# Performance work log

Measured on AMD Instinct MI355X. Metric: run time of the kernel, lower is better.

Reference implementation:

```python
import jax, jax.numpy as jnp
import numpy as np

N = 50000          # nodes
E = 1000000        # edges
EMB = 64           # emb_dim
L = 3              # num_layer
B = 250            # graphs (200 nodes each)
XF, EF = 7, 5      # node / edge feature dims
BN_EPS = 1e-5


def setup_inputs() -> dict:
    key = jax.random.key(0)
    ks = jax.random.split(key, 16)
    x = jax.random.normal(ks[0], (N, XF), dtype=jnp.float32)
    edge_attr = jax.random.normal(ks[1], (E, EF), dtype=jnp.float32)
    edge_index = jax.random.randint(ks[2], (2, E), 0, N, dtype=jnp.int32)
    # 250 contiguous graphs of 200 nodes: last node index of each graph
    last_idx = jnp.arange(1, B + 1, dtype=jnp.int32) * (N // B) - 1
    s = 0.05
    xW = jax.random.normal(ks[3], (XF, EMB), dtype=jnp.float32) * s
    xb = jnp.zeros((EMB,), dtype=jnp.float32)
    eW = jax.random.normal(ks[4], (L, EF, EMB), dtype=jnp.float32) * s
    eb = jnp.zeros((L, EMB), dtype=jnp.float32)
    W1 = jax.random.normal(ks[5], (L, EMB, 2 * EMB), dtype=jnp.float32) * s
    b1 = jnp.zeros((L, 2 * EMB), dtype=jnp.float32)
    W2 = jax.random.normal(ks[6], (L, 2 * EMB, EMB), dtype=jnp.float32) * s
    b2 = jnp.zeros((L, EMB), dtype=jnp.float32)
    gamma = jnp.ones((L, EMB), dtype=jnp.float32)
    beta = jnp.zeros((L, EMB), dtype=jnp.float32)
    return {"x": x, "edge_attr": edge_attr, "edge_index": edge_index,
            "last_idx": last_idx, "xW": xW, "xb": xb, "eW": eW, "eb": eb,
            "W1": W1, "b1": b1, "W2": W2, "b2": b2,
            "gamma": gamma, "beta": beta}


def _gnn_forward(x, edge_attr, edge_index, last_idx, xW, xb, eW, eb, W1, b1, W2, b2, gamma, beta):
    n = x.shape[0]
    # self-loop edge attrs: first column = 8, rest 0
    self_attr = jnp.zeros((n, EF), dtype=edge_attr.dtype).at[:, 0].set(8.0)
    ea = jnp.concatenate([edge_attr, self_attr], axis=0)          # [E+N, EF]
    loop = jnp.arange(n, dtype=edge_index.dtype)
    src = jnp.concatenate([edge_index[0], loop])                  # x_j indices
    dst = jnp.concatenate([edge_index[1], loop])                  # aggregation targets

    h = x @ xW + xb                                               # [N, EMB]
    for l in range(L):
        e = ea @ eW[l] + eb[l]                                    # [E+N, EMB]
        msg = h[src] + e                                          # gather + combine
        agg = jax.ops.segment_sum(msg, dst, num_segments=n)       # scatter-add
        h2 = jax.nn.relu(agg @ W1[l] + b1[l]) @ W2[l] + b2[l]     # GIN MLP
        mean = jnp.mean(h2, axis=0)
        var = jnp.mean(jnp.square(h2 - mean), axis=0)             # biased, like torch BN
        hn = (h2 - mean) * jax.lax.rsqrt(var + BN_EPS) * gamma[l] + beta[l]
        h = jax.nn.elu(hn) if l < L - 1 else hn                   # drop_ratio = 0
    return h[last_idx]                                            # super-node reps [B, EMB]


def reference(x, edge_attr, edge_index, last_idx, xW, xb, eW, eb, W1, b1, W2, b2, gamma, beta):
    return _gnn_forward(x, edge_attr, edge_index, last_idx, xW, xb, eW, eb, W1, b1, W2, b2, gamma, beta)
```

## Files before the change

### kernel.cpp

```cpp
#include <hip/hip_runtime.h>

#define N_NODES 50000
#define N_EDGES 1000000
#define EMB     64
#define HID     128
#define NLAYER  3
#define NGRAPH  250
#define XFD     7
#define EFD     5
#define BN_EPS  1e-5f

#define BKT_SH 8
#define BKT_SZ 256
#define NBKT   ((N_NODES + BKT_SZ - 1) / BKT_SZ)
#define CHKE   4096
#define NCHK   ((N_EDGES + CHKE - 1) / CHKE)
#define CNTM   (NBKT * NCHK)
#define INPB   ((((N_NODES + 1) * EMB) + 255) / 256)
#define PACKB  ((NLAYER * 2 * EMB * HID + 255) / 256)

typedef short bf8_t __attribute__((ext_vector_type(8)));
typedef float f4_t  __attribute__((ext_vector_type(4)));

union FragU {
    uint4 q;
    bf8_t v;
    unsigned short u[8];
};

__device__ __forceinline__ void atomAddF(float* p, float v) {
    __hip_atomic_fetch_add(p, v, __ATOMIC_RELAXED, __HIP_MEMORY_SCOPE_AGENT);
}

__device__ __forceinline__ unsigned short f2bf(float f) {
    unsigned int u = __float_as_uint(f);
    u += 0x7fffu + ((u >> 16) & 1u);
    return (unsigned short)(u >> 16);
}
__device__ __forceinline__ float bf2f(unsigned short s) {
    return __uint_as_float(((unsigned int)s) << 16);
}
__device__ __forceinline__ float4 bf4(ushort4 u) {
    return make_float4(bf2f(u.x), bf2f(u.y), bf2f(u.z), bf2f(u.w));
}

__global__ void k_prep(const float* __restrict__ x, const float* __restrict__ xW,
                       const float* __restrict__ xb, unsigned short* __restrict__ h,
                       const float* __restrict__ W1, const float* __restrict__ W2,
                       unsigned short* __restrict__ pw1, unsigned short* __restrict__ pw2,
                       float* __restrict__ stats) {
    int bid = blockIdx.x;
    if (bid < INPB) {
        int gid = bid * 256 + threadIdx.x;
        if (gid >= (N_NODES + 1) * EMB) return;
        int n = gid >> 6, f = gid & 63;
        if (n == N_NODES) { h[gid] = 0; return; }
        float acc = xb[f];
#pragma unroll
        for (int k = 0; k < XFD; ++k) acc = fmaf(x[n * XFD + k], xW[k * EMB + f], acc);
        h[gid] = f2bf(acc);
    } else if (bid < INPB + PACKB) {
        int gid = (bid - INPB) * 256 + threadIdx.x;
        int layer = gid >> 14;
        int r = gid & 16383;
        if (layer >= NLAYER) return;
        if (r < 8192) {
            int p = r;
            int j = p & 7, lane = (p >> 3) & 63, ts = p >> 9;
            int t = ts >> 1, s = ts & 1;
            int k = 32 * s + 8 * (lane >> 4) + j;
            int n = 16 * t + (lane & 15);
            pw1[layer * 8192 + p] = f2bf(W1[layer * EMB * HID + k * HID + n]);
        } else {
            int p = r - 8192;
            int j = p & 7, lane = (p >> 3) & 63, ts = p >> 9;
            int t = ts >> 2, s = ts & 3;
            int k = 32 * s + 8 * (lane >> 4) + j;
            int n = 16 * t + (lane & 15);
            pw2[layer * 8192 + p] = f2bf(W2[layer * HID * EMB + k * EMB + n]);
        }
    } else {
        for (int i = threadIdx.x; i < NLAYER * 2 * EMB; i += 256) stats[i] = 0.f;
    }
}

__global__ __launch_bounds__(256) void k_binA(const int* __restrict__ dst,
                                              int* __restrict__ cntmat) {
    __shared__ int hist[NBKT];
    int tid = threadIdx.x, c = blockIdx.x;
    for (int i = tid; i < NBKT; i += 256) hist[i] = 0;
    __syncthreads();
    int e0 = c * CHKE, e1 = min(e0 + CHKE, N_EDGES);
    for (int i = e0 + tid; i < e1; i += 256) atomicAdd(&hist[dst[i] >> BKT_SH], 1);
    __syncthreads();
    for (int b = tid; b < NBKT; b += 256) cntmat[b * NCHK + c] = hist[b];
}

__global__ __launch_bounds__(1024) void k_scan(const int* __restrict__ in,
                                               int* __restrict__ out) {
    __shared__ int wsum[16];
    int tid = threadIdx.x, lane = tid & 63, wid = tid >> 6;
    int carry = 0;
    const int4* in4 = (const int4*)in;
    int4* out4 = (int4*)out;
    const int n4 = CNTM / 4;
    for (int base = 0; base < n4; base += 1024) {
        int i = base + tid;
        int4 v = make_int4(0, 0, 0, 0);
        if (i < n4) v = in4[i];
        int t = v.x + v.y + v.z + v.w;
        int x = t;
#pragma unroll
        for (int off = 1; off < 64; off <<= 1) {
            int y = __shfl_up(x, off);
            if (lane >= off) x += y;
        }
        if (lane == 63) wsum[wid] = x;
        __syncthreads();
        int woff = 0, tot = 0;
#pragma unroll
        for (int w = 0; w < 16; ++w) {
            int s = wsum[w];
            if (w < wid) woff += s;
            tot += s;
        }
        if (i < n4) {
            int ex = carry + woff + x - t;
            out4[i] = make_int4(ex, ex + v.x, ex + v.x + v.y, ex + v.x + v.y + v.z);
        }
        carry += tot;
        __syncthreads();
    }
}

__global__ __launch_bounds__(256) void k_binC(const int* __restrict__ src,
                                              const int* __restrict__ dst,
                                              const int* __restrict__ off2,
                                              int2* __restrict__ bufSD) {
    __shared__ int cur[NBKT];
    int tid = threadIdx.x, c = blockIdx.x;
    for (int b = tid; b < NBKT; b += 256) cur[b] = off2[b * NCHK + c];
    __syncthreads();
    int e0 = c * CHKE, e1 = min(e0 + CHKE, N_EDGES);
    for (int i = e0 + tid; i < e1; i += 256) {
        int d = dst[i];
        int b = d >> BKT_SH;
        int p = atomicAdd(&cur[b], 1);
        bufSD[p] = make_int2(src[i], ((d & (BKT_SZ - 1)) << 20) | i);
    }
}

__global__ __launch_bounds__(256) void k_binD(const int2* __restrict__ bufSD,
                                              const int* __restrict__ off2,
                                              int* __restrict__ csr,
                                              int* __restrict__ csrE,
                                              int* __restrict__ rowstart) {
    __shared__ int hist[BKT_SZ];
    __shared__ int cur[BKT_SZ];
    __shared__ int wtot[4];
    int tid = threadIdx.x, b = blockIdx.x;
    int bstart = off2[b * NCHK];
    int bend = (b + 1 < NBKT) ? off2[(b + 1) * NCHK] : N_EDGES;
    hist[tid] = 0;
    __syncthreads();
    for (int j = bstart + tid; j < bend; j += 256)
        atomicAdd(&hist[bufSD[j].y >> 20], 1);
    __syncthreads();
    int lane = tid & 63, wid = tid >> 6;
    int v = hist[tid], x = v;
#pragma unroll
    for (int off = 1; off < 64; off <<= 1) {
        int y = __shfl_up(x, off);
        if (lane >= off) x += y;
    }
    if (lane == 63) wtot[wid] = x;
    __syncthreads();
    int woff = 0;
    for (int w = 0; w < wid; ++w) woff += wtot[w];
    int ex = woff + x - v;
    cur[tid] = ex;
    int node = b * BKT_SZ + tid;
    if (node < N_NODES) rowstart[node] = bstart + ex;
    if (b == NBKT - 1 && tid == 0) rowstart[N_NODES] = N_EDGES;
    __syncthreads();
    for (int j = bstart + tid; j < bend; j += 256) {
        int2 t = bufSD[j];
        int local = t.y >> 20;
        int p = atomicAdd(&cur[local], 1);
        csr[bstart + p] = t.x;
        csrE[bstart + p] = t.y & 0xFFFFF;
    }
}

__global__ __launch_bounds__(256) void k_aggE(const int* __restrict__ rowstart,
                                              const int* __restrict__ csrE,
                                              const float* __restrict__ ea,
                                              float* __restrict__ aggE) {
    int wave = (blockIdx.x * 256 + threadIdx.x) >> 6;
    int lane = threadIdx.x & 63;
    int g = lane >> 4, l15 = lane & 15;
    int n = wave * 4 + g;
    if (n >= N_NODES) return;
    int j0 = rowstart[n], j1 = rowstart[n + 1];
    float s0 = 0.f, s1 = 0.f, s2 = 0.f, s3 = 0.f, s4 = 0.f;
    for (int j = j0 + l15; j < j1; j += 16) {
        int e = csrE[j];
        const float* p = ea + (size_t)e * EFD;
        s0 += p[0]; s1 += p[1]; s2 += p[2]; s3 += p[3]; s4 += p[4];
    }
#pragma unroll
    for (int off = 1; off < 16; off <<= 1) {
        s0 += __shfl_xor(s0, off);
        s1 += __shfl_xor(s1, off);
        s2 += __shfl_xor(s2, off);
        s3 += __shfl_xor(s3, off);
        s4 += __shfl_xor(s4, off);
    }
    if (l15 < 5) {
        float v = (l15 == 0) ? s0 : (l15 == 1) ? s1 : (l15 == 2) ? s2
                : (l15 == 3) ? s3 : s4;
        aggE[(size_t)n * EFD + l15] = v;
    }
}

#define ACC8(v)                                                         \
    do {                                                                \
        f0 += __uint_as_float((v).x << 16);                             \
        f1 += __uint_as_float((v).x & 0xffff0000u);                     \
        f2 += __uint_as_float((v).y << 16);                             \
        f3 += __uint_as_float((v).y & 0xffff0000u);                     \
        f4 += __uint_as_float((v).z << 16);                             \
        f5 += __uint_as_float((v).z & 0xffff0000u);                     \
        f6 += __uint_as_float((v).w << 16);                             \
        f7 += __uint_as_float((v).w & 0xffff0000u);                     \
    } while (0)

__global__ __launch_bounds__(256) void k_agg(const unsigned short* __restrict__ h,
                                             float* __restrict__ agg,
                                             const int* __restrict__ rowstart,
                                             const int* __restrict__ csr,
                                             const float* __restrict__ aggE,
                                             const float* __restrict__ eWl,
                                             const float* __restrict__ ebl) {
    int wave = (blockIdx.x * 256 + threadIdx.x) >> 6;
    int lane = threadIdx.x & 63;
    int nbase = wave * 4;
    if (nbase >= N_NODES) return;
    int lg3 = lane >> 3, lq3 = lane & 7;
    int lg = lane >> 4, lq = lane & 15;
    const uint4* hb8 = (const uint4*)h;
    const ushort4* hb4 = (const ushort4*)h;
    const float4* eW4 = (const float4*)eWl;
    float4 ew0 = eW4[lq], ew1 = eW4[16 + lq], ew2 = eW4[32 + lq],
           ew3 = eW4[48 + lq], ew4 = eW4[64 + lq];
    float4 eb4 = ((const float4*)ebl)[lq];
    int nend = min(nbase + 4, N_NODES);
    for (int n = nbase; n < nend; ++n) {
        int j0 = rowstart[n], j1 = rowstart[n + 1];
        float f0 = 0.f, f1 = 0.f, f2 = 0.f, f3 = 0.f,
              f4 = 0.f, f5 = 0.f, f6 = 0.f, f7 = 0.f;
        for (int j = j0; j < j1;) {
            int take = j1 - j;
            if (take > 64) take = 64;
            int myid = (lane < take) ? csr[j + lane] : N_NODES;
            int s0 = __shfl(myid, lg3);
            int s1 = __shfl(myid, 8 + lg3);
            int s2 = __shfl(myid, 16 + lg3);
            int s3 = __shfl(myid, 24 + lg3);
            uint4 v0 = hb8[(size_t)s0 * 8 + lq3];
            uint4 v1 = hb8[(size_t)s1 * 8 + lq3];
            uint4 v2 = hb8[(size_t)s2 * 8 + lq3];
            uint4 v3 = hb8[(size_t)s3 * 8 + lq3];
            ACC8(v0); ACC8(v1); ACC8(v2); ACC8(v3);
            if (take > 32) {
                int s4 = __shfl(myid, 32 + lg3);
                int s5 = __shfl(myid, 40 + lg3);
                int s6 = __shfl(myid, 48 + lg3);
                int s7 = __shfl(myid, 56 + lg3);
                uint4 w0 = hb8[(size_t)s4 * 8 + lq3];
                uint4 w1 = hb8[(size_t)s5 * 8 + lq3];
                uint4 w2 = hb8[(size_t)s6 * 8 + lq3];
                uint4 w3 = hb8[(size_t)s7 * 8 + lq3];
                ACC8(w0); ACC8(w1); ACC8(w2); ACC8(w3);
            }
            j += take;
        }
#define RED8(F)                     \
        F += __shfl_xor(F, 8);      \
        F += __shfl_xor(F, 16);     \
        F += __shfl_xor(F, 32);
        RED8(f0) RED8(f1) RED8(f2) RED8(f3) RED8(f4) RED8(f5) RED8(f6) RED8(f7)
#undef RED8
        int srcl = lq >> 1;
        float x0 = __shfl(f0, srcl), x4 = __shfl(f4, srcl);
        float x1 = __shfl(f1, srcl), x5 = __shfl(f5, srcl);
        float x2 = __shfl(f2, srcl), x6 = __shfl(f6, srcl);
        float x3 = __shfl(f3, srcl), x7 = __shfl(f7, srcl);
        bool hiHalf = (lq & 1) != 0;
        float4 acc;
        acc.x = hiHalf ? x4 : x0;
        acc.y = hiHalf ? x5 : x1;
        acc.z = hiHalf ? x6 : x2;
        acc.w = hiHalf ? x7 : x3;
        float a0 = aggE[n * 5 + 0], a1 = aggE[n * 5 + 1], a2 = aggE[n * 5 + 2],
              a3 = aggE[n * 5 + 3], a4 = aggE[n * 5 + 4];
        float c0 = a0 + 8.f;
        float ce = (float)(j1 - j0) + 1.f;
        float4 bb = bf4(hb4[(size_t)n * 16 + lq]);
        bb.x = fmaf(c0, ew0.x, bb.x); bb.y = fmaf(c0, ew0.y, bb.y);
        bb.z = fmaf(c0, ew0.z, bb.z); bb.w = fmaf(c0, ew0.w, bb.w);
        bb.x = fmaf(a1, ew1.x, bb.x); bb.y = fmaf(a1, ew1.y, bb.y);
        bb.z = fmaf(a1, ew1.z, bb.z); bb.w = fmaf(a1, ew1.w, bb.w);
        bb.x = fmaf(a2, ew2.x, bb.x); bb.y = fmaf(a2, ew2.y, bb.y);
        bb.z = fmaf(a2, ew2.z, bb.z); bb.w = fmaf(a2, ew2.w, bb.w);
        bb.x = fmaf(a3, ew3.x, bb.x); bb.y = fmaf(a3, ew3.y, bb.y);
        bb.z = fmaf(a3, ew3.z, bb.z); bb.w = fmaf(a3, ew3.w, bb.w);
        bb.x = fmaf(a4, ew4.x, bb.x); bb.y = fmaf(a4, ew4.y, bb.y);
        bb.z = fmaf(a4, ew4.z, bb.z); bb.w = fmaf(a4, ew4.w, bb.w);
        bb.x = fmaf(ce, eb4.x, bb.x); bb.y = fmaf(ce, eb4.y, bb.y);
        bb.z = fmaf(ce, eb4.z, bb.z); bb.w = fmaf(ce, eb4.w, bb.w);
        if (lg == 0) {
            ((float4*)agg)[(size_t)n * 16 + lq] =
                make_float4(acc.x + bb.x, acc.y + bb.y, acc.z + bb.z, acc.w + bb.w);
        }
    }
}
#undef ACC8

__global__ __launch_bounds__(256) void k_mlp(const float* __restrict__ agg,
                                             float* __restrict__ h2,
                                             const unsigned short* __restrict__ pw1,
                                             const float* __restrict__ b1l,
                                             const unsigned short* __restrict__ pw2,
                                             const float* __restrict__ b2l,
                                             float* __restrict__ stats) {
    __shared__ __align__(16) unsigned short hid[64 * 136];
    int tid = threadIdx.x;
    int w = tid >> 6, lane = tid & 63;
    int q = lane >> 4, l15 = lane & 15;
    int n0 = blockIdx.x * 64;
    int mrow = n0 + 16 * w + l15;
    const float* arow = agg + (size_t)(mrow < N_NODES ? mrow : N_NODES - 1) * EMB;
    FragU fa[2];
#pragma unroll
    for (int s = 0; s < 2; ++s) {
        float4 x0 = *(const float4*)&arow[32 * s + 8 * q];
        float4 x1 = *(const float4*)&arow[32 * s + 8 * q + 4];
        fa[s].u[0] = f2bf(x0.x); fa[s].u[1] = f2bf(x0.y);
        fa[s].u[2] = f2bf(x0.z); fa[s].u[3] = f2bf(x0.w);
        fa[s].u[4] = f2bf(x1.x); fa[s].u[5] = f2bf(x1.y);
        fa[s].u[6] = f2bf(x1.z); fa[s].u[7] = f2bf(x1.w);
    }
    const uint4* w1f = (const uint4*)pw1;
    f4_t acc1[8];
#pragma unroll
    for (int t = 0; t < 8; ++t) {
        acc1[t] = (f4_t){0.f, 0.f, 0.f, 0.f};
        FragU b0, b1;
        b0.q = w1f[(t * 2 + 0) * 64 + lane];
        b1.q = w1f[(t * 2 + 1) * 64 + lane];
        acc1[t] = __builtin_amdgcn_mfma_f32_16x16x32_bf16(fa[0].v, b0.v, acc1[t], 0, 0, 0);
        acc1[t] = __builtin_amdgcn_mfma_f32_16x16x32_bf16(fa[1].v, b1.v, acc1[t], 0, 0, 0);
    }
#pragma unroll
    for (int t = 0; t < 8; ++t) {
        int col = 16 * t + l15;
        float bv = b1l[col];
#pragma unroll
        for (int r = 0; r < 4; ++r) {
            int m = 16 * w + q * 4 + r;
            hid[m * 136 + col] = f2bf(fmaxf(acc1[t][r] + bv, 0.f));
        }
    }
    FragU fa2[4];
#pragma unroll
    for (int s = 0; s < 4; ++s)
        fa2[s].q = *(const uint4*)&hid[(16 * w + l15) * 136 + 32 * s + 8 * q];
    const uint4* w2f = (const uint4*)pw2;
    f4_t acc2[4];
#pragma unroll
    for (int t = 0; t < 4; ++t) {
        acc2[t] = (f4_t){0.f, 0.f, 0.f, 0.f};
#pragma unroll
        for (int s = 0; s < 4; ++s) {
            FragU b;
            b.q = w2f[(t * 4 + s) * 64 + lane];
            acc2[t] = __builtin_amdgcn_mfma_f32_16x16x32_bf16(fa2[s].v, b.v, acc2[t], 0, 0, 0);
        }
    }
    float sacc[4] = {0.f, 0.f, 0.f, 0.f}, qacc[4] = {0.f, 0.f, 0.f, 0.f};
#pragma unroll
    for (int t = 0; t < 4; ++t) {
        int col = 16 * t + l15;
        float bv = b2l[col];
#pragma unroll
        for (int r = 0; r < 4; ++r) {
            int nn = n0 + 16 * w + q * 4 + r;
            if (nn < N_NODES) {
                float v = acc2[t][r] + bv;
                h2[(size_t)nn * EMB + col] = v;
                sacc[t] += v;
                qacc[t] = fmaf(v, v, qacc[t]);
            }
        }
    }
#pragma unroll
    for (int t = 0; t < 4; ++t) {
        sacc[t] += __shfl_xor(sacc[t], 16); qacc[t] += __shfl_xor(qacc[t], 16);
        sacc[t] += __shfl_xor(sacc[t], 32); qacc[t] += __shfl_xor(qacc[t], 32);
    }
    __syncthreads();
    float* red = (float*)hid;
    if (q == 0) {
#pragma unroll
        for (int t = 0; t < 4; ++t) {
            red[w * 64 + 16 * t + l15] = sacc[t];
            red[256 + w * 64 + 16 * t + l15] = qacc[t];
        }
    }
    __syncthreads();
    if (tid < 64) {
        float s = red[tid] + red[64 + tid] + red[128 + tid] + red[192 + tid];
        float qq = red[256 + tid] + red[320 + tid] + red[384 + tid] + red[448 + tid];
        atomAddF(&stats[tid], s);
        atomAddF(&stats[64 + tid], qq);
    }
}

__global__ void k_bn(const float* __restrict__ h2, unsigned short* __restrict__ h,
                     const float* __restrict__ stats, const float* __restrict__ gam,
                     const float* __restrict__ bet) {
    int gid = blockIdx.x * 256 + threadIdx.x;
    if (gid >= N_NODES * EMB / 4) return;
    int fq = gid & 15;
    const float invN = 1.f / (float)N_NODES;
    float4 s  = ((const float4*)stats)[fq];
    float4 qs = ((const float4*)(stats + 64))[fq];
    float4 g  = ((const float4*)gam)[fq];
    float4 be = ((const float4*)bet)[fq];
    float4 v  = ((const float4*)h2)[gid];
    ushort4 o;
    float m, var, inv, val;
    m = s.x * invN; var = qs.x * invN - m * m; inv = rsqrtf(var + BN_EPS);
    val = (v.x - m) * inv * g.x + be.x; o.x = f2bf(val > 0.f ? val : expm1f(val));
    m = s.y * invN; var = qs.y * invN - m * m; inv = rsqrtf(var + BN_EPS);
    val = (v.y - m) * inv * g.y + be.y; o.y = f2bf(val > 0.f ? val : expm1f(val));
    m = s.z * invN; var = qs.z * invN - m * m; inv = rsqrtf(var + BN_EPS);
    val = (v.z - m) * inv * g.z + be.z; o.z = f2bf(val > 0.f ? val : expm1f(val));
    m = s.w * invN; var = qs.w * invN - m * m; inv = rsqrtf(var + BN_EPS);
    val = (v.w - m) * inv * g.w + be.w; o.w = f2bf(val > 0.f ? val : expm1f(val));
    ((ushort4*)h)[gid] = o;
}

__global__ void k_bnout(const float* __restrict__ h2, const int* __restrict__ last,
                        const float* __restrict__ stats, const float* __restrict__ gam,
                        const float* __restrict__ bet, float* __restrict__ out) {
    int gid = blockIdx.x * 256 + threadIdx.x;
    if (gid >= NGRAPH * EMB) return;
    int b = gid >> 6, f = gid & 63;
    const float invN = 1.f / (float)N_NODES;
    float mean = stats[f] * invN;
    float var = stats[64 + f] * invN - mean * mean;
    float inv = rsqrtf(var + BN_EPS);
    out[gid] = (h2[last[b] * EMB + f] - mean) * inv * gam[f] + bet[f];
}

extern "C" void kernel_launch(void* const* d_in, const int* in_sizes, int n_in,
                              void* d_out, int out_size, void* d_ws, size_t ws_size,
                              hipStream_t stream) {
    const float* x   = (const float*)d_in[0];
    const float* ea  = (const float*)d_in[1];
    const int*   eidx= (const int*)d_in[2];
    const int*   last= (const int*)d_in[3];
    const float* xW  = (const float*)d_in[4];
    const float* xb  = (const float*)d_in[5];
    const float* eW  = (const float*)d_in[6];
    const float* eb  = (const float*)d_in[7];
    const float* W1  = (const float*)d_in[8];
    const float* b1  = (const float*)d_in[9];
    const float* W2  = (const float*)d_in[10];
    const float* b2  = (const float*)d_in[11];
    const float* gam = (const float*)d_in[12];
    const float* bet = (const float*)d_in[13];
    float* out = (float*)d_out;

    const int* srcI = eidx;
    const int* dstI = eidx + N_EDGES;

    float* hslot  = (float*)d_ws;
    float* agg    = hslot + (N_NODES + 1) * EMB;
    float* aggE   = agg + N_NODES * EMB;
    float* stats  = aggE + N_NODES * EFD;
    int* rowstart = (int*)(stats + NLAYER * 2 * EMB);
    int* csr      = rowstart + N_NODES + 4;
    int* csrE     = csr + N_EDGES;
    int* cntmat   = csrE + N_EDGES;
    int* off2     = cntmat + CNTM;
    unsigned short* pw1 = (unsigned short*)(off2 + CNTM);
    unsigned short* pw2 = pw1 + NLAYER * EMB * HID;
    unsigned short* h = (unsigned short*)hslot;
    int2* bufSD   = (int2*)agg;

    k_prep<<<INPB + PACKB + 1, 256, 0, stream>>>(x, xW, xb, h, W1, W2, pw1, pw2, stats);
    k_binA<<<NCHK, 256, 0, stream>>>(dstI, cntmat);
    k_scan<<<1, 1024, 0, stream>>>(cntmat, off2);
    k_binC<<<NCHK, 256, 0, stream>>>(srcI, dstI, off2, bufSD);
    k_binD<<<NBKT, 256, 0, stream>>>(bufSD, off2, csr, csrE, rowstart);
    k_aggE<<<(N_NODES / 4 * 64 + 255) / 256, 256, 0, stream>>>(rowstart, csrE, ea, aggE);

    const int aggBlocks = ((N_NODES + 3) / 4 * 64 + 255) / 256;
    const int mlpBlocks = (N_NODES + 63) / 64;
    const int bnBlocks  = (N_NODES * EMB / 4 + 255) / 256;
    for (int l = 0; l < NLAYER; ++l) {
        k_agg<<<aggBlocks, 256, 0, stream>>>(
            h, agg, rowstart, csr, aggE, eW + l * EFD * EMB, eb + l * EMB);
        k_mlp<<<mlpBlocks, 256, 0, stream>>>(agg, agg, pw1 + l * EMB * HID, b1 + l * HID,
                                             pw2 + l * HID * EMB, b2 + l * EMB,
                                             stats + l * 2 * EMB);
        if (l < NLAYER - 1) {
            k_bn<<<bnBlocks, 256, 0, stream>>>(
                agg, h, stats + l * 2 * EMB, gam + l * EMB, bet + l * EMB);
        } else {
            k_bnout<<<(NGRAPH * EMB + 255) / 256, 256, 0, stream>>>(
                agg, last, stats + l * 2 * EMB, gam + l * EMB, bet + l * EMB, out);
        }
    }
}
```

Measured before the change: 357.4 us.

## Split neighbor gather into two source-index halves for cache locality

Partitions each CSR row by whether the source node lies in the lower or upper half of the node range, recording a per-node midpoint. Aggregation becomes two kernels, each gathering from only one half of the feature table, to shrink the random-access working set. The second pass adds the edge-feature and self terms and accumulates onto the first pass's partial result, which costs an extra launch, an extra read-modify-write of the aggregate buffer, and more partially filled gather windows.

After: 429.3 us. 1.2x slower.

```diff
diff --git a/kernel.cpp b/kernel.cpp
--- a/kernel.cpp
+++ b/kernel.cpp
@@ -9,6 +9,7 @@
 #define XFD     7
 #define EFD     5
 #define BN_EPS  1e-5f
+#define HALF_N  (N_NODES / 2)
 
 #define BKT_SH 8
 #define BKT_SZ 256
@@ -154,20 +155,26 @@
                                               const int* __restrict__ off2,
                                               int* __restrict__ csr,
                                               int* __restrict__ csrE,
-                                              int* __restrict__ rowstart) {
-    __shared__ int hist[BKT_SZ];
-    __shared__ int cur[BKT_SZ];
+                                              int* __restrict__ rowstart,
+                                              int* __restrict__ rowmid) {
+    __shared__ int hist[2 * BKT_SZ];
+    __shared__ int cur[2 * BKT_SZ];
     __shared__ int wtot[4];
     int tid = threadIdx.x, b = blockIdx.x;
     int bstart = off2[b * NCHK];
     int bend = (b + 1 < NBKT) ? off2[(b + 1) * NCHK] : N_EDGES;
     hist[tid] = 0;
-    __syncthreads();
-    for (int j = bstart + tid; j < bend; j += 256)
-        atomicAdd(&hist[bufSD[j].y >> 20], 1);
+    hist[tid + 256] = 0;
+    __syncthreads();
+    for (int j = bstart + tid; j < bend; j += 256) {
+        int2 t = bufSD[j];
+        int key = ((t.y >> 20) << 1) | (t.x >= HALF_N);
+        atomicAdd(&hist[key], 1);
+    }
     __syncthreads();
     int lane = tid & 63, wid = tid >> 6;
-    int v = hist[tid], x = v;
+    int lo = hist[2 * tid], hi = hist[2 * tid + 1];
+    int v = lo + hi, x = v;
 #pragma unroll
     for (int off = 1; off < 64; off <<= 1) {
         int y = __shfl_up(x, off);
@@ -178,15 +185,19 @@
     int woff = 0;
     for (int w = 0; w < wid; ++w) woff += wtot[w];
     int ex = woff + x - v;
-    cur[tid] = ex;
+    cur[2 * tid] = ex;
+    cur[2 * tid + 1] = ex + lo;
     int node = b * BKT_SZ + tid;
-    if (node < N_NODES) rowstart[node] = bstart + ex;
+    if (node < N_NODES) {
+        rowstart[node] = bstart + ex;
+        rowmid[node] = bstart + ex + lo;
+    }
     if (b == NBKT - 1 && tid == 0) rowstart[N_NODES] = N_EDGES;
     __syncthreads();
     for (int j = bstart + tid; j < bend; j += 256) {
         int2 t = bufSD[j];
-        int local = t.y >> 20;
-        int p = atomicAdd(&cur[local], 1);
+        int key = ((t.y >> 20) << 1) | (t.x >= HALF_N);
+        int p = atomicAdd(&cur[key], 1);
         csr[bstart + p] = t.x;
         csrE[bstart + p] = t.y & 0xFFFFF;
     }
@@ -235,13 +246,83 @@
         f7 += __uint_as_float((v).w & 0xffff0000u);                     \
     } while (0)
 
-__global__ __launch_bounds__(256) void k_agg(const unsigned short* __restrict__ h,
-                                             float* __restrict__ agg,
-                                             const int* __restrict__ rowstart,
-                                             const int* __restrict__ csr,
-                                             const float* __restrict__ aggE,
-                                             const float* __restrict__ eWl,
-                                             const float* __restrict__ ebl) {
+#define GATHER_WINDOWS(J0, J1)                                          \
+    for (int j = (J0); j < (J1);) {                                     \
+        int take = (J1) - j;                                            \
+        if (take > 64) take = 64;                                       \
+        int myid = (lane < take) ? csr[j + lane] : N_NODES;             \
+        int s0 = __shfl(myid, lg3);                                     \
+        int s1 = __shfl(myid, 8 + lg3);                                 \
+        int s2 = __shfl(myid, 16 + lg3);                                \
+        int s3 = __shfl(myid, 24 + lg3);                                \
+        uint4 v0 = hb8[(size_t)s0 * 8 + lq3];                           \
+        uint4 v1 = hb8[(size_t)s1 * 8 + lq3];                           \
+        uint4 v2 = hb8[(size_t)s2 * 8 + lq3];                           \
+        uint4 v3 = hb8[(size_t)s3 * 8 + lq3];                           \
+        ACC8(v0); ACC8(v1); ACC8(v2); ACC8(v3);                         \
+        if (take > 32) {                                                \
+            int s4 = __shfl(myid, 32 + lg3);                            \
+            int s5 = __shfl(myid, 40 + lg3);                            \
+            int s6 = __shfl(myid, 48 + lg3);                            \
+            int s7 = __shfl(myid, 56 + lg3);                            \
+            uint4 w0 = hb8[(size_t)s4 * 8 + lq3];                       \
+            uint4 w1 = hb8[(size_t)s5 * 8 + lq3];                       \
+            uint4 w2 = hb8[(size_t)s6 * 8 + lq3];                       \
+            uint4 w3 = hb8[(size_t)s7 * 8 + lq3];                       \
+            ACC8(w0); ACC8(w1); ACC8(w2); ACC8(w3);                     \
+        }                                                               \
+        j += take;                                                      \
+    }
+
+#define RED8(F)                     \
+    F += __shfl_xor(F, 8);          \
+    F += __shfl_xor(F, 16);         \
+    F += __shfl_xor(F, 32);
+
+__global__ __launch_bounds__(256) void k_aggL(const unsigned short* __restrict__ h,
+                                              float* __restrict__ agg,
+                                              const int* __restrict__ rowstart,
+                                              const int* __restrict__ rowmid,
+                                              const int* __restrict__ csr) {
+    int wave = (blockIdx.x * 256 + threadIdx.x) >> 6;
+    int lane = threadIdx.x & 63;
+    int nbase = wave * 4;
+    if (nbase >= N_NODES) return;
+    int lg3 = lane >> 3, lq3 = lane & 7;
+    int lg = lane >> 4, lq = lane & 15;
+    const uint4* hb8 = (const uint4*)h;
+    int nend = min(nbase + 4, N_NODES);
+    for (int n = nbase; n < nend; ++n) {
+        int j0 = rowstart[n], j1 = rowmid[n];
+        float f0 = 0.f, f1 = 0.f, f2 = 0.f, f3 = 0.f,
+              f4 = 0.f, f5 = 0.f, f6 = 0.f, f7 = 0.f;
+        GATHER_WINDOWS(j0, j1)
+        RED8(f0) RED8(f1) RED8(f2) RED8(f3) RED8(f4) RED8(f5) RED8(f6) RED8(f7)
+        int srcl = lq >> 1;
+        float x0 = __shfl(f0, srcl), x4 = __shfl(f4, srcl);
+        float x1 = __shfl(f1, srcl), x5 = __shfl(f5, srcl);
+        float x2 = __shfl(f2, srcl), x6 = __shfl(f6, srcl);
+        float x3 = __shfl(f3, srcl), x7 = __shfl(f7, srcl);
+        bool hiHalf = (lq & 1) != 0;
+        if (lg == 0) {
+            float4 acc;
+            acc.x = hiHalf ? x4 : x0;
+            acc.y = hiHalf ? x5 : x1;
+            acc.z = hiHalf ? x6 : x2;
+            acc.w = hiHalf ? x7 : x3;
+            ((float4*)agg)[(size_t)n * 16 + lq] = acc;
+        }
+    }
+}
+
+__global__ __launch_bounds__(256) void k_aggH(const unsigned short* __restrict__ h,
+                                              float* __restrict__ agg,
+                                              const int* __restrict__ rowstart,
+                                              const int* __restrict__ rowmid,
+                                              const int* __restrict__ csr,
+                                              const float* __restrict__ aggE,
+                                              const float* __restrict__ eWl,
+                                              const float* __restrict__ ebl) {
     int wave = (blockIdx.x * 256 + threadIdx.x) >> 6;
     int lane = threadIdx.x & 63;
     int nbase = wave * 4;
@@ -256,41 +337,12 @@
     float4 eb4 = ((const float4*)ebl)[lq];
     int nend = min(nbase + 4, N_NODES);
     for (int n = nbase; n < nend; ++n) {
-        int j0 = rowstart[n], j1 = rowstart[n + 1];
+        int jm = rowmid[n], j1 = rowstart[n + 1];
+        int deg = j1 - rowstart[n];
         float f0 = 0.f, f1 = 0.f, f2 = 0.f, f3 = 0.f,
               f4 = 0.f, f5 = 0.f, f6 = 0.f, f7 = 0.f;
-        for (int j = j0; j < j1;) {
-            int take = j1 - j;
-            if (take > 64) take = 64;
-            int myid = (lane < take) ? csr[j + lane] : N_NODES;
-            int s0 = __shfl(myid, lg3);
-            int s1 = __shfl(myid, 8 + lg3);
-            int s2 = __shfl(myid, 16 + lg3);
-            int s3 = __shfl(myid, 24 + lg3);
-            uint4 v0 = hb8[(size_t)s0 * 8 + lq3];
-            uint4 v1 = hb8[(size_t)s1 * 8 + lq3];
-            uint4 v2 = hb8[(size_t)s2 * 8 + lq3];
-            uint4 v3 = hb8[(size_t)s3 * 8 + lq3];
-            ACC8(v0); ACC8(v1); ACC8(v2); ACC8(v3);
-            if (take > 32) {
-                int s4 = __shfl(myid, 32 + lg3);
-                int s5 = __shfl(myid, 40 + lg3);
-                int s6 = __shfl(myid, 48 + lg3);
-                int s7 = __shfl(myid, 56 + lg3);
-                uint4 w0 = hb8[(size_t)s4 * 8 + lq3];
-                uint4 w1 = hb8[(size_t)s5 * 8 + lq3];
-                uint4 w2 = hb8[(size_t)s6 * 8 + lq3];
-                uint4 w3 = hb8[(size_t)s7 * 8 + lq3];
-                ACC8(w0); ACC8(w1); ACC8(w2); ACC8(w3);
-            }
-            j += take;
-        }
-#define RED8(F)                     \
-        F += __shfl_xor(F, 8);      \
-        F += __shfl_xor(F, 16);     \
-        F += __shfl_xor(F, 32);
+        GATHER_WINDOWS(jm, j1)
         RED8(f0) RED8(f1) RED8(f2) RED8(f3) RED8(f4) RED8(f5) RED8(f6) RED8(f7)
-#undef RED8
         int srcl = lq >> 1;
         float x0 = __shfl(f0, srcl), x4 = __shfl(f4, srcl);
         float x1 = __shfl(f1, srcl), x5 = __shfl(f5, srcl);
@@ -305,7 +357,7 @@
         float a0 = aggE[n * 5 + 0], a1 = aggE[n * 5 + 1], a2 = aggE[n * 5 + 2],
               a3 = aggE[n * 5 + 3], a4 = aggE[n * 5 + 4];
         float c0 = a0 + 8.f;
-        float ce = (float)(j1 - j0) + 1.f;
+        float ce = (float)deg + 1.f;
         float4 bb = bf4(hb4[(size_t)n * 16 + lq]);
         bb.x = fmaf(c0, ew0.x, bb.x); bb.y = fmaf(c0, ew0.y, bb.y);
         bb.z = fmaf(c0, ew0.z, bb.z); bb.w = fmaf(c0, ew0.w, bb.w);
@@ -320,11 +372,15 @@
         bb.x = fmaf(ce, eb4.x, bb.x); bb.y = fmaf(ce, eb4.y, bb.y);
         bb.z = fmaf(ce, eb4.z, bb.z); bb.w = fmaf(ce, eb4.w, bb.w);
         if (lg == 0) {
+            float4 prev = ((const float4*)agg)[(size_t)n * 16 + lq];
             ((float4*)agg)[(size_t)n * 16 + lq] =
-                make_float4(acc.x + bb.x, acc.y + bb.y, acc.z + bb.z, acc.w + bb.w);
-        }
-    }
-}
+                make_float4(prev.x + acc.x + bb.x, prev.y + acc.y + bb.y,
+                            prev.z + acc.z + bb.z, prev.w + acc.w + bb.w);
+        }
+    }
+}
+#undef GATHER_WINDOWS
+#undef RED8
 #undef ACC8
 
 __global__ __launch_bounds__(256) void k_mlp(const float* __restrict__ agg,
@@ -492,7 +548,8 @@
     float* aggE   = agg + N_NODES * EMB;
     float* stats  = aggE + N_NODES * EFD;
     int* rowstart = (int*)(stats + NLAYER * 2 * EMB);
-    int* csr      = rowstart + N_NODES + 4;
+    int* rowmid   = rowstart + N_NODES + 4;
+    int* csr      = rowmid + N_NODES + 4;
     int* csrE     = csr + N_EDGES;
     int* cntmat   = csrE + N_EDGES;
     int* off2     = cntmat + CNTM;
@@ -505,15 +562,16 @@
     k_binA<<<NCHK, 256, 0, stream>>>(dstI, cntmat);
     k_scan<<<1, 1024, 0, stream>>>(cntmat, off2);
     k_binC<<<NCHK, 256, 0, stream>>>(srcI, dstI, off2, bufSD);
-    k_binD<<<NBKT, 256, 0, stream>>>(bufSD, off2, csr, csrE, rowstart);
+    k_binD<<<NBKT, 256, 0, stream>>>(bufSD, off2, csr, csrE, rowstart, rowmid);
     k_aggE<<<(N_NODES / 4 * 64 + 255) / 256, 256, 0, stream>>>(rowstart, csrE, ea, aggE);
 
     const int aggBlocks = ((N_NODES + 3) / 4 * 64 + 255) / 256;
     const int mlpBlocks = (N_NODES + 63) / 64;
     const int bnBlocks  = (N_NODES * EMB / 4 + 255) / 256;
     for (int l = 0; l < NLAYER; ++l) {
-        k_agg<<<aggBlocks, 256, 0, stream>>>(
-            h, agg, rowstart, csr, aggE, eW + l * EFD * EMB, eb + l * EMB);
+        k_aggL<<<aggBlocks, 256, 0, stream>>>(h, agg, rowstart, rowmid, csr);
+        k_aggH<<<aggBlocks, 256, 0, stream>>>(
+            h, agg, rowstart, rowmid, csr, aggE, eW + l * EFD * EMB, eb + l * EMB);
         k_mlp<<<mlpBlocks, 256, 0, stream>>>(agg, agg, pw1 + l * EMB * HID, b1 + l * HID,
                                              pw2 + l * HID * EMB, b2 + l * EMB,
                                              stats + l * 2 * EMB);
```

## Fuse neighbor aggregation and GIN MLP into one kernel via LDS staging

Applied to the files above, without the earlier changes.

Merges the aggregation kernel and the MLP kernel into a single per-layer kernel. Each block of 64 nodes aggregates its rows, stores them as bf16 in shared memory, and then runs the MFMA MLP straight from shared memory. This removes the fp32 agg round trip through global memory and one launch per layer. In exchange each wave now handles 16 nodes in sequence, where before a wave covered 4 nodes across many more blocks. That lowers the available parallelism and latency hiding for the gather, and the extra shared memory may reduce occupancy.

Result: slower. 437.7 us (+22.5%).

```diff
diff --git a/kernel.cpp b/kernel.cpp
--- a/kernel.cpp
+++ b/kernel.cpp
@@ -235,122 +235,117 @@
         f7 += __uint_as_float((v).w & 0xffff0000u);                     \
     } while (0)
 
-__global__ __launch_bounds__(256) void k_agg(const unsigned short* __restrict__ h,
-                                             float* __restrict__ agg,
+#define RED8(F)                     \
+    F += __shfl_xor(F, 8);          \
+    F += __shfl_xor(F, 16);         \
+    F += __shfl_xor(F, 32);
+
+#define LDS_A_STRIDE 72
+
+__global__ __launch_bounds__(256) void k_lay(const unsigned short* __restrict__ h,
+                                             float* __restrict__ h2,
                                              const int* __restrict__ rowstart,
                                              const int* __restrict__ csr,
                                              const float* __restrict__ aggE,
                                              const float* __restrict__ eWl,
-                                             const float* __restrict__ ebl) {
-    int wave = (blockIdx.x * 256 + threadIdx.x) >> 6;
-    int lane = threadIdx.x & 63;
-    int nbase = wave * 4;
-    if (nbase >= N_NODES) return;
+                                             const float* __restrict__ ebl,
+                                             const unsigned short* __restrict__ pw1,
+                                             const float* __restrict__ b1l,
+                                             const unsigned short* __restrict__ pw2,
+                                             const float* __restrict__ b2l,
+                                             float* __restrict__ stats) {
+    __shared__ __align__(16) unsigned short lds_a[64 * LDS_A_STRIDE];
+    __shared__ __align__(16) unsigned short hid[64 * 136];
+    int tid = threadIdx.x;
+    int w = tid >> 6, lane = tid & 63;
     int lg3 = lane >> 3, lq3 = lane & 7;
     int lg = lane >> 4, lq = lane & 15;
+    int q = lane >> 4, l15 = lane & 15;
+    int n0 = blockIdx.x * 64;
     const uint4* hb8 = (const uint4*)h;
     const ushort4* hb4 = (const ushort4*)h;
     const float4* eW4 = (const float4*)eWl;
     float4 ew0 = eW4[lq], ew1 = eW4[16 + lq], ew2 = eW4[32 + lq],
            ew3 = eW4[48 + lq], ew4 = eW4[64 + lq];
     float4 eb4 = ((const float4*)ebl)[lq];
-    int nend = min(nbase + 4, N_NODES);
-    for (int n = nbase; n < nend; ++n) {
-        int j0 = rowstart[n], j1 = rowstart[n + 1];
-        float f0 = 0.f, f1 = 0.f, f2 = 0.f, f3 = 0.f,
-              f4 = 0.f, f5 = 0.f, f6 = 0.f, f7 = 0.f;
-        for (int j = j0; j < j1;) {
-            int take = j1 - j;
-            if (take > 64) take = 64;
-            int myid = (lane < take) ? csr[j + lane] : N_NODES;
-            int s0 = __shfl(myid, lg3);
-            int s1 = __shfl(myid, 8 + lg3);
-            int s2 = __shfl(myid, 16 + lg3);
-            int s3 = __shfl(myid, 24 + lg3);
-            uint4 v0 = hb8[(size_t)s0 * 8 + lq3];
-            uint4 v1 = hb8[(size_t)s1 * 8 + lq3];
-            uint4 v2 = hb8[(size_t)s2 * 8 + lq3];
-            uint4 v3 = hb8[(size_t)s3 * 8 + lq3];
-            ACC8(v0); ACC8(v1); ACC8(v2); ACC8(v3);
-            if (take > 32) {
-                int s4 = __shfl(myid, 32 + lg3);
-                int s5 = __shfl(myid, 40 + lg3);
-                int s6 = __shfl(myid, 48 + lg3);
-                int s7 = __shfl(myid, 56 + lg3);
-                uint4 w0 = hb8[(size_t)s4 * 8 + lq3];
-                uint4 w1 = hb8[(size_t)s5 * 8 + lq3];
-                uint4 w2 = hb8[(size_t)s6 * 8 + lq3];
-                uint4 w3 = hb8[(size_t)s7 * 8 + lq3];
-                ACC8(w0); ACC8(w1); ACC8(w2); ACC8(w3);
+
+    for (int i = 0; i < 16; ++i) {
+        int nl = 16 * w + i;
+        int n = n0 + nl;
+        if (n < N_NODES) {
+            int j0 = rowstart[n], j1 = rowstart[n + 1];
+            float f0 = 0.f, f1 = 0.f, f2 = 0.f, f3 = 0.f,
+                  f4 = 0.f, f5 = 0.f, f6 = 0.f, f7 = 0.f;
+            for (int j = j0; j < j1;) {
+                int take = j1 - j;
+                if (take > 64) take = 64;
+                int myid = (lane < take) ? csr[j + lane] : N_NODES;
+                int s0 = __shfl(myid, lg3);
+                int s1 = __shfl(myid, 8 + lg3);
+                int s2 = __shfl(myid, 16 + lg3);
+                int s3 = __shfl(myid, 24 + lg3);
+                uint4 v0 = hb8[(size_t)s0 * 8 + lq3];
+                uint4 v1 = hb8[(size_t)s1 * 8 + lq3];
+                uint4 v2 = hb8[(size_t)s2 * 8 + lq3];
+                uint4 v3 = hb8[(size_t)s3 * 8 + lq3];
+                ACC8(v0); ACC8(v1); ACC8(v2); ACC8(v3);
+                if (take > 32) {
+                    int s4 = __shfl(myid, 32 + lg3);
+                    int s5 = __shfl(myid, 40 + lg3);
+                    int s6 = __shfl(myid, 48 + lg3);
+                    int s7 = __shfl(myid, 56 + lg3);
+                    uint4 w0 = hb8[(size_t)s4 * 8 + lq3];
+                    uint4 w1 = hb8[(size_t)s5 * 8 + lq3];
+                    uint4 w2 = hb8[(size_t)s6 * 8 + lq3];
+                    uint4 w3 = hb8[(size_t)s7 * 8 + lq3];
+                    ACC8(w0); ACC8(w1); ACC8(w2); ACC8(w3);
+                }
+                j += take;
             }
-            j += take;
-        }
-#define RED8(F)                     \
-        F += __shfl_xor(F, 8);      \
-        F += __shfl_xor(F, 16);     \
-        F += __shfl_xor(F, 32);
-        RED8(f0) RED8(f1) RED8(f2) RED8(f3) RED8(f4) RED8(f5) RED8(f6) RED8(f7)
-#undef RED8
-        int srcl = lq >> 1;
-        float x0 = __shfl(f0, srcl), x4 = __shfl(f4, srcl);
-        float x1 = __shfl(f1, srcl), x5 = __shfl(f5, srcl);
-        float x2 = __shfl(f2, srcl), x6 = __shfl(f6, srcl);
-        float x3 = __shfl(f3, srcl), x7 = __shfl(f7, srcl);
-        bool hiHalf = (lq & 1) != 0;
-        float4 acc;
-        acc.x = hiHalf ? x4 : x0;
-        acc.y = hiHalf ? x5 : x1;
-        acc.z = hiHalf ? x6 : x2;
-        acc.w = hiHalf ? x7 : x3;
-        float a0 = aggE[n * 5 + 0], a1 = aggE[n * 5 + 1], a2 = aggE[n * 5 + 2],
-              a3 = aggE[n * 5 + 3], a4 = aggE[n * 5 + 4];
-        float c0 = a0 + 8.f;
-        float ce = (float)(j1 - j0) + 1.f;
-        float4 bb = bf4(hb4[(size_t)n * 16 + lq]);
-        bb.x = fmaf(c0, ew0.x, bb.x); bb.y = fmaf(c0, ew0.y, bb.y);
-        bb.z = fmaf(c0, ew0.z, bb.z); bb.w = fmaf(c0, ew0.w, bb.w);
-        bb.x = fmaf(a1, ew1.x, bb.x); bb.y = fmaf(a1, ew1.y, bb.y);
-        bb.z = fmaf(a1, ew1.z, bb.z); bb.w = fmaf(a1, ew1.w, bb.w);
-        bb.x = fmaf(a2, ew2.x, bb.x); bb.y = fmaf(a2, ew2.y, bb.y);
-        bb.z = fmaf(a2, ew2.z, bb.z); bb.w = fmaf(a2, ew2.w, bb.w);
-        bb.x = fmaf(a3, ew3.x, bb.x); bb.y = fmaf(a3, ew3.y, bb.y);
-        bb.z = fmaf(a3, ew3.z, bb.z); bb.w = fmaf(a3, ew3.w, bb.w);
-        bb.x = fmaf(a4, ew4.x, bb.x); bb.y = fmaf(a4, ew4.y, bb.y);
-        bb.z = fmaf(a4, ew4.z, bb.z); bb.w = fmaf(a4, ew4.w, bb.w);
-        bb.x = fmaf(ce, eb4.x, bb.x); bb.y = fmaf(ce, eb4.y, bb.y);
-        bb.z = fmaf(ce, eb4.z, bb.z); bb.w = fmaf(ce, eb4.w, bb.w);
-        if (lg == 0) {
-            ((float4*)agg)[(size_t)n * 16 + lq] =
-                make_float4(acc.x + bb.x, acc.y + bb.y, acc.z + bb.z, acc.w + bb.w);
-        }
-    }
-}
-#undef ACC8
-
-__global__ __launch_bounds__(256) void k_mlp(const float* __restrict__ agg,
-                                             float* __restrict__ h2,
-                                             const unsigned short* __restrict__ pw1,
-                                             const float* __restrict__ b1l,
-                                             const unsigned short* __restrict__ pw2,
-                                             const float* __restrict__ b2l,
-                                             float* __restrict__ stats) {
-    __shared__ __align__(16) unsigned short hid[64 * 136];
-    int tid = threadIdx.x;
-    int w = tid >> 6, lane = tid & 63;
-    int q = lane >> 4, l15 = lane & 15;
-    int n0 = blockIdx.x * 64;
-    int mrow = n0 + 16 * w + l15;
-    const float* arow = agg + (size_t)(mrow < N_NODES ? mrow : N_NODES - 1) * EMB;
+            RED8(f0) RED8(f1) RED8(f2) RED8(f3) RED8(f4) RED8(f5) RED8(f6) RED8(f7)
+            int srcl = lq >> 1;
+            float x0 = __shfl(f0, srcl), x4 = __shfl(f4, srcl);
+            float x1 = __shfl(f1, srcl), x5 = __shfl(f5, srcl);
+            float x2 = __shfl(f2, srcl), x6 = __shfl(f6, srcl);
+            float x3 = __shfl(f3, srcl), x7 = __shfl(f7, srcl);
+            bool hiHalf = (lq & 1) != 0;
+            float4 acc;
+            acc.x = hiHalf ? x4 : x0;
+            acc.y = hiHalf ? x5 : x1;
+            acc.z = hiHalf ? x6 : x2;
+            acc.w = hiHalf ? x7 : x3;
+            float a0 = aggE[n * 5 + 0], a1 = aggE[n * 5 + 1], a2 = aggE[n * 5 + 2],
+                  a3 = aggE[n * 5 + 3], a4 = aggE[n * 5 + 4];
+            float c0 = a0 + 8.f;
+            float ce = (float)(j1 - j0) + 1.f;
+            float4 bb = bf4(hb4[(size_t)n * 16 + lq]);
+            bb.x = fmaf(c0, ew0.x, bb.x); bb.y = fmaf(c0, ew0.y, bb.y);
+            bb.z = fmaf(c0, ew0.z, bb.z); bb.w = fmaf(c0, ew0.w, bb.w);
+            bb.x = fmaf(a1, ew1.x, bb.x); bb.y = fmaf(a1, ew1.y, bb.y);
+            bb.z = fmaf(a1, ew1.z, bb.z); bb.w = fmaf(a1, ew1.w, bb.w);
+            bb.x = fmaf(a2, ew2.x, bb.x); bb.y = fmaf(a2, ew2.y, bb.y);
+            bb.z = fmaf(a2, ew2.z, bb.z); bb.w = fmaf(a2, ew2.w, bb.w);
+            bb.x = fmaf(a3, ew3.x, bb.x); bb.y = fmaf(a3, ew3.y, bb.y);
+            bb.z = fmaf(a3, ew3.z, bb.z); bb.w = fmaf(a3, ew3.w, bb.w);
+            bb.x = fmaf(a4, ew4.x, bb.x); bb.y = fmaf(a4, ew4.y, bb.y);
+            bb.z = fmaf(a4, ew4.z, bb.z); bb.w = fmaf(a4, ew4.w, bb.w);
+            bb.x = fmaf(ce, eb4.x, bb.x); bb.y = fmaf(ce, eb4.y, bb.y);
+            bb.z = fmaf(ce, eb4.z, bb.z); bb.w = fmaf(ce, eb4.w, bb.w);
+            if (lg == 0) {
+                ushort4 o;
+                o.x = f2bf(acc.x + bb.x); o.y = f2bf(acc.y + bb.y);
+                o.z = f2bf(acc.z + bb.z); o.w = f2bf(acc.w + bb.w);
+                *(ushort4*)&lds_a[nl * LDS_A_STRIDE + 4 * lq] = o;
+            }
+        } else if (lg == 0) {
+            *(ushort4*)&lds_a[nl * LDS_A_STRIDE + 4 * lq] = make_ushort4(0, 0, 0, 0);
+        }
+    }
+
     FragU fa[2];
 #pragma unroll
-    for (int s = 0; s < 2; ++s) {
-        float4 x0 = *(const float4*)&arow[32 * s + 8 * q];
-        float4 x1 = *(const float4*)&arow[32 * s + 8 * q + 4];
-        fa[s].u[0] = f2bf(x0.x); fa[s].u[1] = f2bf(x0.y);
-        fa[s].u[2] = f2bf(x0.z); fa[s].u[3] = f2bf(x0.w);
-        fa[s].u[4] = f2bf(x1.x); fa[s].u[5] = f2bf(x1.y);
-        fa[s].u[6] = f2bf(x1.z); fa[s].u[7] = f2bf(x1.w);
-    }
+    for (int s = 0; s < 2; ++s)
+        fa[s].q = *(const uint4*)&lds_a[(16 * w + l15) * LDS_A_STRIDE + 32 * s + 8 * q];
     const uint4* w1f = (const uint4*)pw1;
     f4_t acc1[8];
 #pragma unroll
@@ -426,6 +421,8 @@
         atomAddF(&stats[64 + tid], qq);
     }
 }
+#undef ACC8
+#undef RED8
 
 __global__ void k_bn(const float* __restrict__ h2, unsigned short* __restrict__ h,
                      const float* __restrict__ stats, const float* __restrict__ gam,
@@ -488,8 +485,8 @@
     const int* dstI = eidx + N_EDGES;
 
     float* hslot  = (float*)d_ws;
-    float* agg    = hslot + (N_NODES + 1) * EMB;
-    float* aggE   = agg + N_NODES * EMB;
+    float* h2buf  = hslot + (N_NODES + 1) * EMB;
+    float* aggE   = h2buf + N_NODES * EMB;
     float* stats  = aggE + N_NODES * EFD;
     int* rowstart = (int*)(stats + NLAYER * 2 * EMB);
     int* csr      = rowstart + N_NODES + 4;
@@ -499,7 +496,7 @@
     unsigned short* pw1 = (unsigned short*)(off2 + CNTM);
     unsigned short* pw2 = pw1 + NLAYER * EMB * HID;
     unsigned short* h = (unsigned short*)hslot;
-    int2* bufSD   = (int2*)agg;
+    int2* bufSD   = (int2*)h2buf;
 
     k_prep<<<INPB + PACKB + 1, 256, 0, stream>>>(x, xW, xb, h, W1, W2, pw1, pw2, stats);
     k_binA<<<NCHK, 256, 0, stream>>>(dstI, cntmat);
@@ -508,21 +505,19 @@
     k_binD<<<NBKT, 256, 0, stream>>>(bufSD, off2, csr, csrE, rowstart);
     k_aggE<<<(N_NODES / 4 * 64 + 255) / 256, 256, 0, stream>>>(rowstart, csrE, ea, aggE);
 
-    const int aggBlocks = ((N_NODES + 3) / 4 * 64 + 255) / 256;
-    const int mlpBlocks = (N_NODES + 63) / 64;
+    const int layBlocks = (N_NODES + 63) / 64;
     const int bnBlocks  = (N_NODES * EMB / 4 + 255) / 256;
     for (int l = 0; l < NLAYER; ++l) {
-        k_agg<<<aggBlocks, 256, 0, stream>>>(
-            h, agg, rowstart, csr, aggE, eW + l * EFD * EMB, eb + l * EMB);
-        k_mlp<<<mlpBlocks, 256, 0, stream>>>(agg, agg, pw1 + l * EMB * HID, b1 + l * HID,
-                                             pw2 + l * HID * EMB, b2 + l * EMB,
-                                             stats + l * 2 * EMB);
+        k_lay<<<layBlocks, 256, 0, stream>>>(
+            h, h2buf, rowstart, csr, aggE, eW + l * EFD * EMB, eb + l * EMB,
+            pw1 + l * EMB * HID, b1 + l * HID, pw2 + l * HID * EMB, b2 + l * EMB,
+            stats + l * 2 * EMB);
         if (l < NLAYER - 1) {
             k_bn<<<bnBlocks, 256, 0, stream>>>(
-                agg, h, stats + l * 2 * EMB, gam + l * EMB, bet + l * EMB);
+                h2buf, h, stats + l * 2 * EMB, gam + l * EMB, bet + l * EMB);
         } else {
             k_bnout<<<(NGRAPH * EMB + 255) / 256, 256, 0, stream>>>(
-                agg, last, stats + l * 2 * EMB, gam + l * EMB, bet + l * EMB, out);
-        }
-    }
-}
+                h2buf, last, stats + l * 2 * EMB, gam + l * EMB, bet + l * EMB, out);
+        }
+    }
+}
```
